# Performance work log

Hardware: AMD Instinct MI355X
Metric: run time of the kernel (lower is better)

Reference implementation:

```python
import jax, jax.numpy as jnp
import numpy as np

B, S, D = 1, 2048, 2048
H, KV, HD = 16, 4, 128
HALF = HD // 2
REP = H // KV
LAMBDA_INIT = 0.5
OUT_SCALE = 1.0 - LAMBDA_INIT


def _rope(x, cos, sin):
    # x: (B, S, heads, HD); cos/sin: (S, HD//2). Complex pair rotation on
    # interleaved (even, odd) channels, matching torch.view_as_complex.
    orig_shape = x.shape
    xp = x.reshape(*x.shape[:-1], -1, 2)
    x0, x1 = xp[..., 0], xp[..., 1]
    c = cos[None, :, None, :]
    s = sin[None, :, None, :]
    r0 = x0 * c - x1 * s
    r1 = x0 * s + x1 * c
    return jnp.stack([r0, r1], axis=-1).reshape(orig_shape)


def _sdpa_causal(q, k, v, scale):
    # q,k: (B, S, H, half), v: (B, S, H, HD). Causal softmax attention.
    scores = jnp.einsum('bshd,bthd->bhst', q, k) * scale
    causal = jnp.tril(jnp.ones((S, S), dtype=bool))
    scores = jnp.where(causal[None, None, :, :], scores, jnp.finfo(scores.dtype).min)
    p = jax.nn.softmax(scores, axis=-1)
    return jnp.einsum('bhst,bthd->bshd', p, v)


def setup_inputs() -> dict:
    key = jax.random.key(0)
    ks = jax.random.split(key, 7)
    x = jax.random.normal(ks[0], (B, S, D), dtype=jnp.float32)
    # RoPE frequencies: theta_i = 10000^(-2i/HD), angles = pos * theta
    inv_freq = 1.0 / (10000.0 ** (np.arange(0, HD, 2, dtype=np.float32) / HD))
    angles = np.arange(S, dtype=np.float32)[:, None] * inv_freq[None, :]
    freqs_cos = jnp.asarray(np.cos(angles), dtype=jnp.float32)
    freqs_sin = jnp.asarray(np.sin(angles), dtype=jnp.float32)
    sd = 0.02
    Wq = jax.random.normal(ks[1], (D, H * HD), dtype=jnp.float32) * sd
    Wk = jax.random.normal(ks[2], (D, KV * HD), dtype=jnp.float32) * sd
    Wv = jax.random.normal(ks[3], (D, KV * HD), dtype=jnp.float32) * sd
    Wo = jax.random.normal(ks[4], (H * HD, D), dtype=jnp.float32) * sd
    lam0 = float(np.log(LAMBDA_INIT / (1.0 - LAMBDA_INIT)))
    lambda_param = jnp.full((H,), lam0, dtype=jnp.float32)
    return {'x': x, 'freqs_cos': freqs_cos, 'freqs_sin': freqs_sin,
            'Wq': Wq, 'Wk': Wk, 'Wv': Wv, 'Wo': Wo, 'lambda_param': lambda_param}


def reference(x, freqs_cos, freqs_sin, Wq, Wk, Wv, Wo, lambda_param):
    q = (x @ Wq).reshape(B, S, H, HD)
    k = (x @ Wk).reshape(B, S, KV, HD)
    v = (x @ Wv).reshape(B, S, KV, HD)
    q = _rope(q, freqs_cos, freqs_sin)
    k = _rope(k, freqs_cos, freqs_sin)
    # GQA expansion: each kv head repeated REP times consecutively
    k = jnp.repeat(k, REP, axis=2)
    v = jnp.repeat(v, REP, axis=2)
    q1, q2 = q[..., :HALF], q[..., HALF:]
    k1, k2 = k[..., :HALF], k[..., HALF:]
    scale = 1.0 / jnp.sqrt(jnp.float32(HALF))  # SDPA scales by query last dim
    a1 = _sdpa_causal(q1, k1, v, scale)  # (B, S, H, HD)
    a2 = _sdpa_causal(q2, k2, v, scale)
    lam = jax.nn.sigmoid(lambda_param).astype(x.dtype)[None, None, :, None]
    out = (a1 - lam * a2) * OUT_SCALE
    out = out.reshape(B, S, H * HD)
    return out @ Wo
```

## Files before the change

kernel.cpp:

```cpp
#include <hip/hip_runtime.h>
#include <hip/hip_bf16.h>
#include <cstdint>

typedef __bf16 bf16_t;
typedef __attribute__((ext_vector_type(8))) __bf16 bf16x8;
typedef __attribute__((ext_vector_type(4))) __bf16 bf16x4;
typedef __attribute__((ext_vector_type(4))) float f32x4;

#define S_LEN 2048
#define D_MODEL 2048
#define NH 16
#define NKV 4
#define HD_ 128

#define MFMA16(a, b, c) __builtin_amdgcn_mfma_f32_16x16x32_bf16((a), (b), (c), 0, 0, 0)

__device__ __forceinline__ void gload_lds16(const void* g, void* l) {
  __builtin_amdgcn_global_load_lds((__attribute__((address_space(1))) void*)((void*)g),
                                   (__attribute__((address_space(3))) void*)(l), 16, 0, 0);
}

__global__ __launch_bounds__(256) void cast_x_kernel(const float* __restrict__ in,
                                                     bf16_t* __restrict__ out, int n4) {
  int i = blockIdx.x * 256 + threadIdx.x;
  if (i >= n4) return;
  float4 v = reinterpret_cast<const float4*>(in)[i];
  bf16x4 o = {(__bf16)v.x, (__bf16)v.y, (__bf16)v.z, (__bf16)v.w};
  *reinterpret_cast<bf16x4*>(out + (size_t)i * 4) = o;
}

__global__ void transpose_cast_kernel(const float* __restrict__ in, bf16_t* __restrict__ out,
                                      int ldin, int ldout) {
  __shared__ float t[32][33];
  int c0 = blockIdx.x * 32, r0 = blockIdx.y * 32;
  int x = threadIdx.x, y = threadIdx.y;
  t[y][x] = in[(size_t)(r0 + y) * ldin + (c0 + x)];
  __syncthreads();
  out[(size_t)(c0 + y) * ldout + (r0 + x)] = (__bf16)t[x][y];
}

__global__ __launch_bounds__(256) void rope_q_kernel(const float* __restrict__ qkv,
    const float* __restrict__ cosT, const float* __restrict__ sinT, bf16_t* __restrict__ Qb) {
  int s = blockIdx.x;
#pragma unroll
  for (int i = 0; i < 4; ++i) {
    int p = i * 256 + threadIdx.x;
    int h = p >> 6, j = p & 63;
    float c = cosT[s * 64 + j], sn = sinT[s * 64 + j];
    const float* src = qkv + (size_t)s * 3072 + h * 128 + 2 * j;
    float x0 = src[0], x1 = src[1];
    bf16_t* dst = Qb + ((size_t)h * S_LEN + s) * HD_ + 2 * j;
    dst[0] = (__bf16)(x0 * c - x1 * sn);
    dst[1] = (__bf16)(x0 * sn + x1 * c);
  }
}

__global__ __launch_bounds__(256) void rope_k_kernel(const float* __restrict__ qkv,
    const float* __restrict__ cosT, const float* __restrict__ sinT, bf16_t* __restrict__ Kb) {
  int s = blockIdx.x;
  int p = threadIdx.x;
  int kv = p >> 6, j = p & 63;
  float c = cosT[s * 64 + j], sn = sinT[s * 64 + j];
  const float* src = qkv + (size_t)s * 3072 + 2048 + kv * 128 + 2 * j;
  float x0 = src[0], x1 = src[1];
  bf16_t* dst = Kb + ((size_t)kv * S_LEN + s) * HD_ + 2 * j;
  dst[0] = (__bf16)(x0 * c - x1 * sn);
  dst[1] = (__bf16)(x0 * sn + x1 * c);
}

#define BM 128
#define BN 128
#define BK 64

__global__ __launch_bounds__(256) void gemm_bf16_kernel(const bf16_t* __restrict__ A,
    const bf16_t* __restrict__ B, float* __restrict__ C, int M, int N, int K) {
  __shared__ __attribute__((aligned(16))) bf16_t aL[BM * BK];
  __shared__ __attribute__((aligned(16))) bf16_t bL[BN * BK];
  const int tid = threadIdx.x;
  const int wave = tid >> 6, lane = tid & 63;
  const int wr = wave >> 1, wc = wave & 1;
  const int l15 = lane & 15, l4 = lane >> 4;
  const int bm = blockIdx.y * BM, bn = blockIdx.x * BN;

  f32x4 zero = {0.f, 0.f, 0.f, 0.f};
  f32x4 acc[4][4];
#pragma unroll
  for (int m = 0; m < 4; ++m)
#pragma unroll
    for (int n = 0; n < 4; ++n) acc[m][n] = zero;

  const bf16_t* aSrc[4];
  const bf16_t* bSrc[4];
  bf16_t* aDst[4];
  bf16_t* bDst[4];
#pragma unroll
  for (int i = 0; i < 4; ++i) {
    int ci = i * 256 + tid;
    int r = ci >> 3;
    int cl = (ci & 7) ^ (r & 7);
    aSrc[i] = A + (size_t)(bm + r) * K + cl * 8;
    bSrc[i] = B + (size_t)(bn + r) * K + cl * 8;
    aDst[i] = aL + (i * 256 + wave * 64) * 8;
    bDst[i] = bL + (i * 256 + wave * 64) * 8;
  }

  for (int kt = 0; kt < K; kt += BK) {
#pragma unroll
    for (int i = 0; i < 4; ++i) gload_lds16(aSrc[i] + kt, aDst[i]);
#pragma unroll
    for (int i = 0; i < 4; ++i) gload_lds16(bSrc[i] + kt, bDst[i]);
    __syncthreads();
#pragma unroll
    for (int t = 0; t < 2; ++t) {
      bf16x8 af[4], bfr[4];
#pragma unroll
      for (int f = 0; f < 4; ++f) {
        int Ra = wr * 64 + f * 16 + l15;
        int ca = (t * 4 + l4) ^ (Ra & 7);
        af[f] = *reinterpret_cast<const bf16x8*>(aL + Ra * 64 + ca * 8);
        int Rb = wc * 64 + f * 16 + l15;
        int cb = (t * 4 + l4) ^ (Rb & 7);
        bfr[f] = *reinterpret_cast<const bf16x8*>(bL + Rb * 64 + cb * 8);
      }
#pragma unroll
      for (int m = 0; m < 4; ++m)
#pragma unroll
        for (int n = 0; n < 4; ++n) acc[m][n] = MFMA16(af[m], bfr[n], acc[m][n]);
    }
    __syncthreads();
  }

#pragma unroll
  for (int m = 0; m < 4; ++m) {
    int row0 = bm + wr * 64 + m * 16 + l4 * 4;
#pragma unroll
    for (int n = 0; n < 4; ++n) {
      int col = bn + wc * 64 + n * 16 + l15;
#pragma unroll
      for (int r = 0; r < 4; ++r) C[(size_t)(row0 + r) * N + col] = acc[m][n][r];
    }
  }
}

#define P_PITCH 72

__global__ __launch_bounds__(256) void diff_attn_kernel(const bf16_t* __restrict__ Qb,
    const bf16_t* __restrict__ Kb, const bf16_t* __restrict__ VTb,
    const float* __restrict__ lambda_param, bf16_t* __restrict__ attn) {
  const int h = blockIdx.y;
  const int kvh = h >> 2;
  const int pr = blockIdx.x;
  const int tid = threadIdx.x, wave = tid >> 6, lane = tid & 63;
  const int l15 = lane & 15, l4 = lane >> 4;

  __shared__ __attribute__((aligned(16))) bf16_t kB[2][64 * 128];
  __shared__ __attribute__((aligned(16))) bf16_t vB[2][64 * 128];
  __shared__ __attribute__((aligned(16))) bf16_t pS[4][2][16 * P_PITCH];

  const bf16_t* kBase = Kb + (size_t)kvh * S_LEN * HD_;
  const bf16_t* vBase = VTb + (size_t)kvh * HD_ * S_LEN;
  int kOff[4], vOff[4], dOff[4];
#pragma unroll
  for (int i = 0; i < 4; ++i) {
    int ci = i * 256 + tid;
    int kr = ci >> 4;
    kOff[i] = kr * HD_ + (((ci & 15) ^ (kr & 7)) * 8);
    int vr = ci >> 3;
    vOff[i] = vr * S_LEN + (((ci & 7) ^ (vr & 7)) * 8);
    dOff[i] = (i * 256 + wave * 64) * 8;
  }

  const float SC = 0.18033688f;
  const float lam = 1.f / (1.f + __expf(-lambda_param[h]));
  const f32x4 zero = {0.f, 0.f, 0.f, 0.f};

  for (int ph = 0; ph < 2; ++ph) {
    const int jt = (ph == 0) ? pr : 31 - pr;
    const int q0 = jt * 64;
    const int qg = q0 + wave * 16 + l15;

    const bf16_t* qp = Qb + ((size_t)h * S_LEN + qg) * HD_;
    bf16x8 qf[4];
#pragma unroll
    for (int f = 0; f < 4; ++f) qf[f] = *reinterpret_cast<const bf16x8*>(qp + f * 32 + l4 * 8);

    f32x4 o1[8], o2[8];
#pragma unroll
    for (int n = 0; n < 8; ++n) { o1[n] = zero; o2[n] = zero; }
    float m1 = -__builtin_inff(), m2 = -__builtin_inff(), l1 = 0.f, l2 = 0.f;

#pragma unroll
    for (int i = 0; i < 4; ++i) gload_lds16(kBase + kOff[i], &kB[0][0] + dOff[i]);
#pragma unroll
    for (int i = 0; i < 4; ++i) gload_lds16(vBase + vOff[i], &vB[0][0] + dOff[i]);
    __syncthreads();

    for (int t = 0; t <= jt; ++t) {
      const int cur = t & 1;
      if (t < jt) {
        const size_t kv0n = (size_t)(t + 1) * 64;
#pragma unroll
        for (int i = 0; i < 4; ++i) gload_lds16(kBase + kv0n * HD_ + kOff[i], &kB[cur ^ 1][0] + dOff[i]);
#pragma unroll
        for (int i = 0; i < 4; ++i) gload_lds16(vBase + kv0n + vOff[i], &vB[cur ^ 1][0] + dOff[i]);
      }
      const bf16_t* kL = &kB[cur][0];
      const bf16_t* vL = &vB[cur][0];
      const int kv0 = t * 64;

      f32x4 s1[4], s2[4];
#pragma unroll
      for (int n = 0; n < 4; ++n) { s1[n] = zero; s2[n] = zero; }
#pragma unroll
      for (int tt = 0; tt < 2; ++tt) {
#pragma unroll
        for (int n = 0; n < 4; ++n) {
          const int Rk = n * 16 + l15;
          bf16x8 kf1 = *reinterpret_cast<const bf16x8*>(kL + Rk * 128 + (((tt * 4 + l4) ^ (Rk & 7)) * 8));
          s1[n] = MFMA16(kf1, qf[tt], s1[n]);
        }
      }
#pragma unroll
      for (int tt = 0; tt < 2; ++tt) {
#pragma unroll
        for (int n = 0; n < 4; ++n) {
          const int Rk = n * 16 + l15;
          bf16x8 kf2 = *reinterpret_cast<const bf16x8*>(kL + Rk * 128 + (((8 + tt * 4 + l4) ^ (Rk & 7)) * 8));
          s2[n] = MFMA16(kf2, qf[2 + tt], s2[n]);
        }
      }

      const bool diag = (t == jt);
#pragma unroll
      for (int n = 0; n < 4; ++n)
#pragma unroll
        for (int r = 0; r < 4; ++r) {
          float v1 = s1[n][r] * SC, v2 = s2[n][r] * SC;
          if (diag && (kv0 + n * 16 + l4 * 4 + r > qg)) { v1 = -1e30f; v2 = -1e30f; }
          s1[n][r] = v1; s2[n][r] = v2;
        }

      float sc1, sc2;
      {
        float tmax = -3.4e38f;
#pragma unroll
        for (int n = 0; n < 4; ++n)
#pragma unroll
          for (int r = 0; r < 4; ++r) tmax = fmaxf(tmax, s1[n][r]);
        tmax = fmaxf(tmax, __shfl_xor(tmax, 16));
        tmax = fmaxf(tmax, __shfl_xor(tmax, 32));
        const float mn = fmaxf(m1, tmax);
        sc1 = __builtin_exp2f(m1 - mn);
        m1 = mn;
        float rs = 0.f;
#pragma unroll
        for (int n = 0; n < 4; ++n) {
          float e0 = __builtin_exp2f(s1[n][0] - mn);
          float e1 = __builtin_exp2f(s1[n][1] - mn);
          float e2 = __builtin_exp2f(s1[n][2] - mn);
          float e3 = __builtin_exp2f(s1[n][3] - mn);
          rs += (e0 + e1) + (e2 + e3);
          bf16x4 pk = {(__bf16)e0, (__bf16)e1, (__bf16)e2, (__bf16)e3};
          *reinterpret_cast<bf16x4*>(&pS[wave][0][l15 * P_PITCH + n * 16 + l4 * 4]) = pk;
        }
        rs += __shfl_xor(rs, 16);
        rs += __shfl_xor(rs, 32);
        l1 = l1 * sc1 + rs;
      }
      {
        float tmax = -3.4e38f;
#pragma unroll
        for (int n = 0; n < 4; ++n)
#pragma unroll
          for (int r = 0; r < 4; ++r) tmax = fmaxf(tmax, s2[n][r]);
        tmax = fmaxf(tmax, __shfl_xor(tmax, 16));
        tmax = fmaxf(tmax, __shfl_xor(tmax, 32));
        const float mn = fmaxf(m2, tmax);
        sc2 = __builtin_exp2f(m2 - mn);
        m2 = mn;
        float rs = 0.f;
#pragma unroll
        for (int n = 0; n < 4; ++n) {
          float e0 = __builtin_exp2f(s2[n][0] - mn);
          float e1 = __builtin_exp2f(s2[n][1] - mn);
          float e2 = __builtin_exp2f(s2[n][2] - mn);
          float e3 = __builtin_exp2f(s2[n][3] - mn);
          rs += (e0 + e1) + (e2 + e3);
          bf16x4 pk = {(__bf16)e0, (__bf16)e1, (__bf16)e2, (__bf16)e3};
          *reinterpret_cast<bf16x4*>(&pS[wave][1][l15 * P_PITCH + n * 16 + l4 * 4]) = pk;
        }
        rs += __shfl_xor(rs, 16);
        rs += __shfl_xor(rs, 32);
        l2 = l2 * sc2 + rs;
      }
#pragma unroll
      for (int n = 0; n < 8; ++n) { o1[n] *= sc1; o2[n] *= sc2; }

#pragma unroll
      for (int kt = 0; kt < 2; ++kt) {
        bf16x8 pf1 = *reinterpret_cast<const bf16x8*>(&pS[wave][0][l15 * P_PITCH + kt * 32 + l4 * 8]);
        bf16x8 pf2 = *reinterpret_cast<const bf16x8*>(&pS[wave][1][l15 * P_PITCH + kt * 32 + l4 * 8]);
#pragma unroll
        for (int n = 0; n < 8; ++n) {
          const int Rv = n * 16 + l15;
          bf16x8 vf = *reinterpret_cast<const bf16x8*>(vL + Rv * 64 + (((kt * 4 + l4) ^ (Rv & 7)) * 8));
          o1[n] = MFMA16(vf, pf1, o1[n]);
          o2[n] = MFMA16(vf, pf2, o2[n]);
        }
      }
      __syncthreads();
    }

    const float i1 = 1.f / l1, i2 = lam / l2;
    bf16_t* orow = attn + (size_t)qg * D_MODEL + h * HD_;
#pragma unroll
    for (int n = 0; n < 8; ++n) {
      bf16x4 w = {(__bf16)((o1[n][0] * i1 - o2[n][0] * i2) * 0.5f),
                  (__bf16)((o1[n][1] * i1 - o2[n][1] * i2) * 0.5f),
                  (__bf16)((o1[n][2] * i1 - o2[n][2] * i2) * 0.5f),
                  (__bf16)((o1[n][3] * i1 - o2[n][3] * i2) * 0.5f)};
      *reinterpret_cast<bf16x4*>(orow + n * 16 + l4 * 4) = w;
    }
  }
}

extern "C" void kernel_launch(void* const* d_in, const int* in_sizes, int n_in,
                              void* d_out, int out_size, void* d_ws, size_t ws_size,
                              hipStream_t stream) {
  const float* x    = (const float*)d_in[0];
  const float* fcos = (const float*)d_in[1];
  const float* fsin = (const float*)d_in[2];
  const float* Wq   = (const float*)d_in[3];
  const float* Wk   = (const float*)d_in[4];
  const float* Wv   = (const float*)d_in[5];
  const float* Wo   = (const float*)d_in[6];
  const float* lam  = (const float*)d_in[7];
  float* out = (float*)d_out;

  char* w = (char*)d_ws;
  bf16_t* xb    = (bf16_t*)(w);
  bf16_t* attnb = (bf16_t*)(w);
  bf16_t* WqkvT = (bf16_t*)(w + (8ull << 20));
  bf16_t* Qb    = (bf16_t*)(w + (8ull << 20));
  bf16_t* Kb    = (bf16_t*)(w + (16ull << 20));
  bf16_t* VT    = (bf16_t*)(w + (18ull << 20));
  bf16_t* WoT   = (bf16_t*)(w + (20ull << 20));
  float*  QKV   = (float*) (w + (28ull << 20));

  dim3 tb(32, 32);
  cast_x_kernel<<<4096, 256, 0, stream>>>(x, xb, 1048576);
  transpose_cast_kernel<<<dim3(64, 64), tb, 0, stream>>>(Wq, WqkvT, 2048, 2048);
  transpose_cast_kernel<<<dim3(16, 64), tb, 0, stream>>>(Wk, WqkvT + 2048 * 2048, 512, 2048);
  transpose_cast_kernel<<<dim3(16, 64), tb, 0, stream>>>(Wv, WqkvT + 2560 * 2048, 512, 2048);
  transpose_cast_kernel<<<dim3(64, 64), tb, 0, stream>>>(Wo, WoT, 2048, 2048);

  gemm_bf16_kernel<<<dim3(24, 16), 256, 0, stream>>>(xb, WqkvT, QKV, 2048, 3072, 2048);

  rope_q_kernel<<<2048, 256, 0, stream>>>(QKV, fcos, fsin, Qb);
  rope_k_kernel<<<2048, 256, 0, stream>>>(QKV, fcos, fsin, Kb);
  transpose_cast_kernel<<<dim3(16, 64), tb, 0, stream>>>(QKV + 2560, VT, 3072, 2048);

  diff_attn_kernel<<<dim3(16, 16), 256, 0, stream>>>(Qb, Kb, VT, lam, attnb);

  gemm_bf16_kernel<<<dim3(16, 16), 256, 0, stream>>>(attnb, WoT, out, 2048, 2048, 2048);
}
```

Before: 299.5 us.

## Rework attention grid, lazy softmax rescale, vectorized transpose/cast and fused RoPE

Attention now launches one block per (head, query tile) instead of pairing two tiles per block, with the longest tiles scheduled first. The softmax only rescales the accumulators when the running max grows by more than 8. The Q scale is folded into RoPE, and the P buffer uses an XOR swizzle instead of padding. The prep kernels are rewritten to use 64x64 vectorized transpose-cast, 8-wide casts and a single fused Q/K RoPE kernel. Together these aim to raise occupancy and load balance and to cut prep launches and uncoalesced memory traffic, at the cost of more blocks and a slightly looser numeric bound on the exponentials.

```diff
diff --git a/kernel.cpp b/kernel.cpp
--- a/kernel.cpp
+++ b/kernel.cpp
@@ -21,51 +21,83 @@
 }
 
 __global__ __launch_bounds__(256) void cast_x_kernel(const float* __restrict__ in,
-                                                     bf16_t* __restrict__ out, int n4) {
+                                                     bf16_t* __restrict__ out, int n8) {
   int i = blockIdx.x * 256 + threadIdx.x;
-  if (i >= n4) return;
-  float4 v = reinterpret_cast<const float4*>(in)[i];
-  bf16x4 o = {(__bf16)v.x, (__bf16)v.y, (__bf16)v.z, (__bf16)v.w};
-  *reinterpret_cast<bf16x4*>(out + (size_t)i * 4) = o;
-}
-
-__global__ void transpose_cast_kernel(const float* __restrict__ in, bf16_t* __restrict__ out,
-                                      int ldin, int ldout) {
-  __shared__ float t[32][33];
-  int c0 = blockIdx.x * 32, r0 = blockIdx.y * 32;
-  int x = threadIdx.x, y = threadIdx.y;
-  t[y][x] = in[(size_t)(r0 + y) * ldin + (c0 + x)];
+  if (i >= n8) return;
+  float4 a = reinterpret_cast<const float4*>(in)[2 * i];
+  float4 b = reinterpret_cast<const float4*>(in)[2 * i + 1];
+  bf16x8 o = {(__bf16)a.x, (__bf16)a.y, (__bf16)a.z, (__bf16)a.w,
+              (__bf16)b.x, (__bf16)b.y, (__bf16)b.z, (__bf16)b.w};
+  *reinterpret_cast<bf16x8*>(out + (size_t)i * 8) = o;
+}
+
+__global__ __launch_bounds__(256) void transpose_cast64_kernel(const float* __restrict__ in,
+    bf16_t* __restrict__ out, int ldin, int ldout) {
+  __shared__ float t[64][65];
+  const int c0 = blockIdx.x * 64, r0 = blockIdx.y * 64;
+  const int rr = threadIdx.x >> 4;
+  const int cc = (threadIdx.x & 15) * 4;
+#pragma unroll
+  for (int p = 0; p < 4; ++p) {
+    int r = rr + p * 16;
+    float4 v = *reinterpret_cast<const float4*>(in + (size_t)(r0 + r) * ldin + c0 + cc);
+    t[r][cc] = v.x; t[r][cc + 1] = v.y; t[r][cc + 2] = v.z; t[r][cc + 3] = v.w;
+  }
   __syncthreads();
-  out[(size_t)(c0 + y) * ldout + (r0 + x)] = (__bf16)t[x][y];
-}
-
-__global__ __launch_bounds__(256) void rope_q_kernel(const float* __restrict__ qkv,
-    const float* __restrict__ cosT, const float* __restrict__ sinT, bf16_t* __restrict__ Qb) {
-  int s = blockIdx.x;
-#pragma unroll
-  for (int i = 0; i < 4; ++i) {
-    int p = i * 256 + threadIdx.x;
-    int h = p >> 6, j = p & 63;
-    float c = cosT[s * 64 + j], sn = sinT[s * 64 + j];
-    const float* src = qkv + (size_t)s * 3072 + h * 128 + 2 * j;
-    float x0 = src[0], x1 = src[1];
-    bf16_t* dst = Qb + ((size_t)h * S_LEN + s) * HD_ + 2 * j;
-    dst[0] = (__bf16)(x0 * c - x1 * sn);
-    dst[1] = (__bf16)(x0 * sn + x1 * c);
-  }
-}
-
-__global__ __launch_bounds__(256) void rope_k_kernel(const float* __restrict__ qkv,
-    const float* __restrict__ cosT, const float* __restrict__ sinT, bf16_t* __restrict__ Kb) {
-  int s = blockIdx.x;
-  int p = threadIdx.x;
-  int kv = p >> 6, j = p & 63;
-  float c = cosT[s * 64 + j], sn = sinT[s * 64 + j];
-  const float* src = qkv + (size_t)s * 3072 + 2048 + kv * 128 + 2 * j;
-  float x0 = src[0], x1 = src[1];
-  bf16_t* dst = Kb + ((size_t)kv * S_LEN + s) * HD_ + 2 * j;
-  dst[0] = (__bf16)(x0 * c - x1 * sn);
-  dst[1] = (__bf16)(x0 * sn + x1 * c);
+  const int c = threadIdx.x >> 2;
+  const int q = threadIdx.x & 3;
+  bf16_t* orow = out + (size_t)(c0 + c) * ldout + r0 + q * 16;
+#pragma unroll
+  for (int half = 0; half < 2; ++half) {
+    bf16x8 o;
+#pragma unroll
+    for (int j = 0; j < 8; ++j) o[j] = (__bf16)t[q * 16 + half * 8 + j][c];
+    *reinterpret_cast<bf16x8*>(orow + half * 8) = o;
+  }
+}
+
+#define SC_Q 0.18033688f
+
+__global__ __launch_bounds__(256) void rope_kernel(const float* __restrict__ qkv,
+    const float* __restrict__ cosT, const float* __restrict__ sinT,
+    bf16_t* __restrict__ Qb, bf16_t* __restrict__ Kb) {
+  const int s = blockIdx.x;
+  const int tid = threadIdx.x;
+  const int ch = tid & 15;
+  float4 cs = *reinterpret_cast<const float4*>(cosT + s * 64 + ch * 4);
+  float4 sn = *reinterpret_cast<const float4*>(sinT + s * 64 + ch * 4);
+  {
+    const int hq = tid >> 4;
+    const float* src = qkv + (size_t)s * 3072 + hq * 128 + ch * 8;
+    float4 a = *reinterpret_cast<const float4*>(src);
+    float4 b = *reinterpret_cast<const float4*>(src + 4);
+    bf16x8 o;
+    o[0] = (__bf16)((a.x * cs.x - a.y * sn.x) * SC_Q);
+    o[1] = (__bf16)((a.x * sn.x + a.y * cs.x) * SC_Q);
+    o[2] = (__bf16)((a.z * cs.y - a.w * sn.y) * SC_Q);
+    o[3] = (__bf16)((a.z * sn.y + a.w * cs.y) * SC_Q);
+    o[4] = (__bf16)((b.x * cs.z - b.y * sn.z) * SC_Q);
+    o[5] = (__bf16)((b.x * sn.z + b.y * cs.z) * SC_Q);
+    o[6] = (__bf16)((b.z * cs.w - b.w * sn.w) * SC_Q);
+    o[7] = (__bf16)((b.z * sn.w + b.w * cs.w) * SC_Q);
+    *reinterpret_cast<bf16x8*>(Qb + ((size_t)hq * S_LEN + s) * HD_ + ch * 8) = o;
+  }
+  if (tid < 64) {
+    const int kh = tid >> 4;
+    const float* src = qkv + (size_t)s * 3072 + 2048 + kh * 128 + ch * 8;
+    float4 a = *reinterpret_cast<const float4*>(src);
+    float4 b = *reinterpret_cast<const float4*>(src + 4);
+    bf16x8 o;
+    o[0] = (__bf16)(a.x * cs.x - a.y * sn.x);
+    o[1] = (__bf16)(a.x * sn.x + a.y * cs.x);
+    o[2] = (__bf16)(a.z * cs.y - a.w * sn.y);
+    o[3] = (__bf16)(a.z * sn.y + a.w * cs.y);
+    o[4] = (__bf16)(b.x * cs.z - b.y * sn.z);
+    o[5] = (__bf16)(b.x * sn.z + b.y * cs.z);
+    o[6] = (__bf16)(b.z * cs.w - b.w * sn.w);
+    o[7] = (__bf16)(b.z * sn.w + b.w * cs.w);
+    *reinterpret_cast<bf16x8*>(Kb + ((size_t)kh * S_LEN + s) * HD_ + ch * 8) = o;
+  }
 }
 
 #define BM 128
@@ -142,20 +174,18 @@
   }
 }
 
-#define P_PITCH 72
-
 __global__ __launch_bounds__(256) void diff_attn_kernel(const bf16_t* __restrict__ Qb,
     const bf16_t* __restrict__ Kb, const bf16_t* __restrict__ VTb,
     const float* __restrict__ lambda_param, bf16_t* __restrict__ attn) {
-  const int h = blockIdx.y;
+  const int h = blockIdx.x;
   const int kvh = h >> 2;
-  const int pr = blockIdx.x;
+  const int jt = (blockIdx.y < 16) ? (31 - blockIdx.y) : (blockIdx.y - 16);
   const int tid = threadIdx.x, wave = tid >> 6, lane = tid & 63;
   const int l15 = lane & 15, l4 = lane >> 4;
 
   __shared__ __attribute__((aligned(16))) bf16_t kB[2][64 * 128];
   __shared__ __attribute__((aligned(16))) bf16_t vB[2][64 * 128];
-  __shared__ __attribute__((aligned(16))) bf16_t pS[4][2][16 * P_PITCH];
+  __shared__ __attribute__((aligned(16))) bf16_t pS[4][2][16 * 64];
 
   const bf16_t* kBase = Kb + (size_t)kvh * S_LEN * HD_;
   const bf16_t* vBase = VTb + (size_t)kvh * HD_ * S_LEN;
@@ -170,157 +200,161 @@
     dOff[i] = (i * 256 + wave * 64) * 8;
   }
 
-  const float SC = 0.18033688f;
   const float lam = 1.f / (1.f + __expf(-lambda_param[h]));
   const f32x4 zero = {0.f, 0.f, 0.f, 0.f};
 
-  for (int ph = 0; ph < 2; ++ph) {
-    const int jt = (ph == 0) ? pr : 31 - pr;
-    const int q0 = jt * 64;
-    const int qg = q0 + wave * 16 + l15;
-
-    const bf16_t* qp = Qb + ((size_t)h * S_LEN + qg) * HD_;
-    bf16x8 qf[4];
-#pragma unroll
-    for (int f = 0; f < 4; ++f) qf[f] = *reinterpret_cast<const bf16x8*>(qp + f * 32 + l4 * 8);
-
-    f32x4 o1[8], o2[8];
-#pragma unroll
-    for (int n = 0; n < 8; ++n) { o1[n] = zero; o2[n] = zero; }
-    float m1 = -__builtin_inff(), m2 = -__builtin_inff(), l1 = 0.f, l2 = 0.f;
-
-#pragma unroll
-    for (int i = 0; i < 4; ++i) gload_lds16(kBase + kOff[i], &kB[0][0] + dOff[i]);
-#pragma unroll
-    for (int i = 0; i < 4; ++i) gload_lds16(vBase + vOff[i], &vB[0][0] + dOff[i]);
+  const int q0 = jt * 64;
+  const int qg = q0 + wave * 16 + l15;
+
+  const bf16_t* qp = Qb + ((size_t)h * S_LEN + qg) * HD_;
+  bf16x8 qf[4];
+#pragma unroll
+  for (int f = 0; f < 4; ++f) qf[f] = *reinterpret_cast<const bf16x8*>(qp + f * 32 + l4 * 8);
+
+  f32x4 o1[8], o2[8];
+#pragma unroll
+  for (int n = 0; n < 8; ++n) { o1[n] = zero; o2[n] = zero; }
+  float m1 = -__builtin_inff(), m2 = -__builtin_inff(), l1 = 0.f, l2 = 0.f;
+
+#pragma unroll
+  for (int i = 0; i < 4; ++i) gload_lds16(kBase + kOff[i], &kB[0][0] + dOff[i]);
+#pragma unroll
+  for (int i = 0; i < 4; ++i) gload_lds16(vBase + vOff[i], &vB[0][0] + dOff[i]);
+  __syncthreads();
+
+  for (int t = 0; t <= jt; ++t) {
+    const int cur = t & 1;
+    if (t < jt) {
+      const size_t kv0n = (size_t)(t + 1) * 64;
+#pragma unroll
+      for (int i = 0; i < 4; ++i) gload_lds16(kBase + kv0n * HD_ + kOff[i], &kB[cur ^ 1][0] + dOff[i]);
+#pragma unroll
+      for (int i = 0; i < 4; ++i) gload_lds16(vBase + kv0n + vOff[i], &vB[cur ^ 1][0] + dOff[i]);
+    }
+    const bf16_t* kL = &kB[cur][0];
+    const bf16_t* vL = &vB[cur][0];
+    const int kv0 = t * 64;
+
+    f32x4 s1[4], s2[4];
+#pragma unroll
+    for (int n = 0; n < 4; ++n) { s1[n] = zero; s2[n] = zero; }
+#pragma unroll
+    for (int tt = 0; tt < 2; ++tt) {
+#pragma unroll
+      for (int n = 0; n < 4; ++n) {
+        const int Rk = n * 16 + l15;
+        bf16x8 kf1 = *reinterpret_cast<const bf16x8*>(kL + Rk * 128 + (((tt * 4 + l4) ^ (Rk & 7)) * 8));
+        s1[n] = MFMA16(kf1, qf[tt], s1[n]);
+      }
+    }
+#pragma unroll
+    for (int tt = 0; tt < 2; ++tt) {
+#pragma unroll
+      for (int n = 0; n < 4; ++n) {
+        const int Rk = n * 16 + l15;
+        bf16x8 kf2 = *reinterpret_cast<const bf16x8*>(kL + Rk * 128 + (((8 + tt * 4 + l4) ^ (Rk & 7)) * 8));
+        s2[n] = MFMA16(kf2, qf[2 + tt], s2[n]);
+      }
+    }
+
+    if (t == jt) {
+#pragma unroll
+      for (int n = 0; n < 4; ++n)
+#pragma unroll
+        for (int r = 0; r < 4; ++r)
+          if (kv0 + n * 16 + l4 * 4 + r > qg) { s1[n][r] = -1e30f; s2[n][r] = -1e30f; }
+    }
+
+    {
+      float tmax = s1[0][0];
+#pragma unroll
+      for (int n = 0; n < 4; ++n)
+#pragma unroll
+        for (int r = 0; r < 4; ++r) tmax = fmaxf(tmax, s1[n][r]);
+      tmax = fmaxf(tmax, __shfl_xor(tmax, 16));
+      tmax = fmaxf(tmax, __shfl_xor(tmax, 32));
+      if (!__all(tmax <= m1 + 8.f)) {
+        const float mn = fmaxf(m1, tmax);
+        const float sc = __builtin_exp2f(m1 - mn);
+        m1 = mn;
+        l1 *= sc;
+#pragma unroll
+        for (int n = 0; n < 8; ++n) o1[n] *= sc;
+      }
+      float rs = 0.f;
+#pragma unroll
+      for (int n = 0; n < 4; ++n) {
+        float e0 = __builtin_exp2f(s1[n][0] - m1);
+        float e1 = __builtin_exp2f(s1[n][1] - m1);
+        float e2 = __builtin_exp2f(s1[n][2] - m1);
+        float e3 = __builtin_exp2f(s1[n][3] - m1);
+        rs += (e0 + e1) + (e2 + e3);
+        int cswz = (n * 2 + (l4 >> 1)) ^ (l15 & 7);
+        bf16x4 pk = {(__bf16)e0, (__bf16)e1, (__bf16)e2, (__bf16)e3};
+        *reinterpret_cast<bf16x4*>(&pS[wave][0][l15 * 64 + cswz * 8 + (l4 & 1) * 4]) = pk;
+      }
+      rs += __shfl_xor(rs, 16);
+      rs += __shfl_xor(rs, 32);
+      l1 += rs;
+    }
+    {
+      float tmax = s2[0][0];
+#pragma unroll
+      for (int n = 0; n < 4; ++n)
+#pragma unroll
+        for (int r = 0; r < 4; ++r) tmax = fmaxf(tmax, s2[n][r]);
+      tmax = fmaxf(tmax, __shfl_xor(tmax, 16));
+      tmax = fmaxf(tmax, __shfl_xor(tmax, 32));
+      if (!__all(tmax <= m2 + 8.f)) {
+        const float mn = fmaxf(m2, tmax);
+        const float sc = __builtin_exp2f(m2 - mn);
+        m2 = mn;
+        l2 *= sc;
+#pragma unroll
+        for (int n = 0; n < 8; ++n) o2[n] *= sc;
+      }
+      float rs = 0.f;
+#pragma unroll
+      for (int n = 0; n < 4; ++n) {
+        float e0 = __builtin_exp2f(s2[n][0] - m2);
+        float e1 = __builtin_exp2f(s2[n][1] - m2);
+        float e2 = __builtin_exp2f(s2[n][2] - m2);
+        float e3 = __builtin_exp2f(s2[n][3] - m2);
+        rs += (e0 + e1) + (e2 + e3);
+        int cswz = (n * 2 + (l4 >> 1)) ^ (l15 & 7);
+        bf16x4 pk = {(__bf16)e0, (__bf16)e1, (__bf16)e2, (__bf16)e3};
+        *reinterpret_cast<bf16x4*>(&pS[wave][1][l15 * 64 + cswz * 8 + (l4 & 1) * 4]) = pk;
+      }
+      rs += __shfl_xor(rs, 16);
+      rs += __shfl_xor(rs, 32);
+      l2 += rs;
+    }
+
+#pragma unroll
+    for (int kt = 0; kt < 2; ++kt) {
+      int cp = ((kt * 4 + l4) ^ (l15 & 7)) * 8;
+      bf16x8 pf1 = *reinterpret_cast<const bf16x8*>(&pS[wave][0][l15 * 64 + cp]);
+      bf16x8 pf2 = *reinterpret_cast<const bf16x8*>(&pS[wave][1][l15 * 64 + cp]);
+#pragma unroll
+      for (int n = 0; n < 8; ++n) {
+        const int Rv = n * 16 + l15;
+        bf16x8 vf = *reinterpret_cast<const bf16x8*>(vL + Rv * 64 + (((kt * 4 + l4) ^ (Rv & 7)) * 8));
+        o1[n] = MFMA16(vf, pf1, o1[n]);
+        o2[n] = MFMA16(vf, pf2, o2[n]);
+      }
+    }
     __syncthreads();
-
-    for (int t = 0; t <= jt; ++t) {
-      const int cur = t & 1;
-      if (t < jt) {
-        const size_t kv0n = (size_t)(t + 1) * 64;
-#pragma unroll
-        for (int i = 0; i < 4; ++i) gload_lds16(kBase + kv0n * HD_ + kOff[i], &kB[cur ^ 1][0] + dOff[i]);
-#pragma unroll
-        for (int i = 0; i < 4; ++i) gload_lds16(vBase + kv0n + vOff[i], &vB[cur ^ 1][0] + dOff[i]);
-      }
-      const bf16_t* kL = &kB[cur][0];
-      const bf16_t* vL = &vB[cur][0];
-      const int kv0 = t * 64;
-
-      f32x4 s1[4], s2[4];
-#pragma unroll
-      for (int n = 0; n < 4; ++n) { s1[n] = zero; s2[n] = zero; }
-#pragma unroll
-      for (int tt = 0; tt < 2; ++tt) {
-#pragma unroll
-        for (int n = 0; n < 4; ++n) {
-          const int Rk = n * 16 + l15;
-          bf16x8 kf1 = *reinterpret_cast<const bf16x8*>(kL + Rk * 128 + (((tt * 4 + l4) ^ (Rk & 7)) * 8));
-          s1[n] = MFMA16(kf1, qf[tt], s1[n]);
-        }
-      }
-#pragma unroll
-      for (int tt = 0; tt < 2; ++tt) {
-#pragma unroll
-        for (int n = 0; n < 4; ++n) {
-          const int Rk = n * 16 + l15;
-          bf16x8 kf2 = *reinterpret_cast<const bf16x8*>(kL + Rk * 128 + (((8 + tt * 4 + l4) ^ (Rk & 7)) * 8));
-          s2[n] = MFMA16(kf2, qf[2 + tt], s2[n]);
-        }
-      }
-
-      const bool diag = (t == jt);
-#pragma unroll
-      for (int n = 0; n < 4; ++n)
-#pragma unroll
-        for (int r = 0; r < 4; ++r) {
-          float v1 = s1[n][r] * SC, v2 = s2[n][r] * SC;
-          if (diag && (kv0 + n * 16 + l4 * 4 + r > qg)) { v1 = -1e30f; v2 = -1e30f; }
-          s1[n][r] = v1; s2[n][r] = v2;
-        }
-
-      float sc1, sc2;
-      {
-        float tmax = -3.4e38f;
-#pragma unroll
-        for (int n = 0; n < 4; ++n)
-#pragma unroll
-          for (int r = 0; r < 4; ++r) tmax = fmaxf(tmax, s1[n][r]);
-        tmax = fmaxf(tmax, __shfl_xor(tmax, 16));
-        tmax = fmaxf(tmax, __shfl_xor(tmax, 32));
-        const float mn = fmaxf(m1, tmax);
-        sc1 = __builtin_exp2f(m1 - mn);
-        m1 = mn;
-        float rs = 0.f;
-#pragma unroll
-        for (int n = 0; n < 4; ++n) {
-          float e0 = __builtin_exp2f(s1[n][0] - mn);
-          float e1 = __builtin_exp2f(s1[n][1] - mn);
-          float e2 = __builtin_exp2f(s1[n][2] - mn);
-          float e3 = __builtin_exp2f(s1[n][3] - mn);
-          rs += (e0 + e1) + (e2 + e3);
-          bf16x4 pk = {(__bf16)e0, (__bf16)e1, (__bf16)e2, (__bf16)e3};
-          *reinterpret_cast<bf16x4*>(&pS[wave][0][l15 * P_PITCH + n * 16 + l4 * 4]) = pk;
-        }
-        rs += __shfl_xor(rs, 16);
-        rs += __shfl_xor(rs, 32);
-        l1 = l1 * sc1 + rs;
-      }
-      {
-        float tmax = -3.4e38f;
-#pragma unroll
-        for (int n = 0; n < 4; ++n)
-#pragma unroll
-          for (int r = 0; r < 4; ++r) tmax = fmaxf(tmax, s2[n][r]);
-        tmax = fmaxf(tmax, __shfl_xor(tmax, 16));
-        tmax = fmaxf(tmax, __shfl_xor(tmax, 32));
-        const float mn = fmaxf(m2, tmax);
-        sc2 = __builtin_exp2f(m2 - mn);
-        m2 = mn;
-        float rs = 0.f;
-#pragma unroll
-        for (int n = 0; n < 4; ++n) {
-          float e0 = __builtin_exp2f(s2[n][0] - mn);
-          float e1 = __builtin_exp2f(s2[n][1] - mn);
-          float e2 = __builtin_exp2f(s2[n][2] - mn);
-          float e3 = __builtin_exp2f(s2[n][3] - mn);
-          rs += (e0 + e1) + (e2 + e3);
-          bf16x4 pk = {(__bf16)e0, (__bf16)e1, (__bf16)e2, (__bf16)e3};
-          *reinterpret_cast<bf16x4*>(&pS[wave][1][l15 * P_PITCH + n * 16 + l4 * 4]) = pk;
-        }
-        rs += __shfl_xor(rs, 16);
-        rs += __shfl_xor(rs, 32);
-        l2 = l2 * sc2 + rs;
-      }
-#pragma unroll
-      for (int n = 0; n < 8; ++n) { o1[n] *= sc1; o2[n] *= sc2; }
-
-#pragma unroll
-      for (int kt = 0; kt < 2; ++kt) {
-        bf16x8 pf1 = *reinterpret_cast<const bf16x8*>(&pS[wave][0][l15 * P_PITCH + kt * 32 + l4 * 8]);
-        bf16x8 pf2 = *reinterpret_cast<const bf16x8*>(&pS[wave][1][l15 * P_PITCH + kt * 32 + l4 * 8]);
-#pragma unroll
-        for (int n = 0; n < 8; ++n) {
-          const int Rv = n * 16 + l15;
-          bf16x8 vf = *reinterpret_cast<const bf16x8*>(vL + Rv * 64 + (((kt * 4 + l4) ^ (Rv & 7)) * 8));
-          o1[n] = MFMA16(vf, pf1, o1[n]);
-          o2[n] = MFMA16(vf, pf2, o2[n]);
-        }
-      }
-      __syncthreads();
-    }
-
-    const float i1 = 1.f / l1, i2 = lam / l2;
-    bf16_t* orow = attn + (size_t)qg * D_MODEL + h * HD_;
-#pragma unroll
-    for (int n = 0; n < 8; ++n) {
-      bf16x4 w = {(__bf16)((o1[n][0] * i1 - o2[n][0] * i2) * 0.5f),
-                  (__bf16)((o1[n][1] * i1 - o2[n][1] * i2) * 0.5f),
-                  (__bf16)((o1[n][2] * i1 - o2[n][2] * i2) * 0.5f),
-                  (__bf16)((o1[n][3] * i1 - o2[n][3] * i2) * 0.5f)};
-      *reinterpret_cast<bf16x4*>(orow + n * 16 + l4 * 4) = w;
-    }
+  }
+
+  const float i1 = 1.f / l1, i2 = lam / l2;
+  bf16_t* orow = attn + (size_t)qg * D_MODEL + h * HD_;
+#pragma unroll
+  for (int n = 0; n < 8; ++n) {
+    bf16x4 w = {(__bf16)((o1[n][0] * i1 - o2[n][0] * i2) * 0.5f),
+                (__bf16)((o1[n][1] * i1 - o2[n][1] * i2) * 0.5f),
+                (__bf16)((o1[n][2] * i1 - o2[n][2] * i2) * 0.5f),
+                (__bf16)((o1[n][3] * i1 - o2[n][3] * i2) * 0.5f)};
+    *reinterpret_cast<bf16x4*>(orow + n * 16 + l4 * 4) = w;
   }
 }
 
@@ -347,20 +381,18 @@
   bf16_t* WoT   = (bf16_t*)(w + (20ull << 20));
   float*  QKV   = (float*) (w + (28ull << 20));
 
-  dim3 tb(32, 32);
-  cast_x_kernel<<<4096, 256, 0, stream>>>(x, xb, 1048576);
-  transpose_cast_kernel<<<dim3(64, 64), tb, 0, stream>>>(Wq, WqkvT, 2048, 2048);
-  transpose_cast_kernel<<<dim3(16, 64), tb, 0, stream>>>(Wk, WqkvT + 2048 * 2048, 512, 2048);
-  transpose_cast_kernel<<<dim3(16, 64), tb, 0, stream>>>(Wv, WqkvT + 2560 * 2048, 512, 2048);
-  transpose_cast_kernel<<<dim3(64, 64), tb, 0, stream>>>(Wo, WoT, 2048, 2048);
+  cast_x_kernel<<<2048, 256, 0, stream>>>(x, xb, 524288);
+  transpose_cast64_kernel<<<dim3(32, 32), 256, 0, stream>>>(Wq, WqkvT, 2048, 2048);
+  transpose_cast64_kernel<<<dim3(8, 32), 256, 0, stream>>>(Wk, WqkvT + 2048 * 2048, 512, 2048);
+  transpose_cast64_kernel<<<dim3(8, 32), 256, 0, stream>>>(Wv, WqkvT + 2560 * 2048, 512, 2048);
+  transpose_cast64_kernel<<<dim3(32, 32), 256, 0, stream>>>(Wo, WoT, 2048, 2048);
 
   gemm_bf16_kernel<<<dim3(24, 16), 256, 0, stream>>>(xb, WqkvT, QKV, 2048, 3072, 2048);
 
-  rope_q_kernel<<<2048, 256, 0, stream>>>(QKV, fcos, fsin, Qb);
-  rope_k_kernel<<<2048, 256, 0, stream>>>(QKV, fcos, fsin, Kb);
-  transpose_cast_kernel<<<dim3(16, 64), tb, 0, stream>>>(QKV + 2560, VT, 3072, 2048);
-
-  diff_attn_kernel<<<dim3(16, 16), 256, 0, stream>>>(Qb, Kb, VT, lam, attnb);
+  rope_kernel<<<2048, 256, 0, stream>>>(QKV, fcos, fsin, Qb, Kb);
+  transpose_cast64_kernel<<<dim3(8, 32), 256, 0, stream>>>(QKV + 2560, VT, 3072, 2048);
+
+  diff_attn_kernel<<<dim3(16, 32), 256, 0, stream>>>(Qb, Kb, VT, lam, attnb);
 
   gemm_bf16_kernel<<<dim3(16, 16), 256, 0, stream>>>(attnb, WoT, out, 2048, 2048, 2048);
 }
```

Result: slower. 306.9 us (+2.5%).
